# Performance work log

Hardware: AMD Instinct MI355X
Metric: run time of the kernel (lower is better)

Reference implementation:

```python
import jax, jax.numpy as jnp
import numpy as np

EPS = 1e-5

def _ln(x):
    # LayerNorm over last dim, no affine (elementwise_affine=False)
    mu = jnp.mean(x, axis=-1, keepdims=True)
    var = jnp.mean(jnp.square(x - mu), axis=-1, keepdims=True)
    return (x - mu) * jax.lax.rsqrt(var + EPS)

def setup_inputs() -> dict:
    key = jax.random.key(0)
    ks = jax.random.split(key, 6)
    B, L, D = 2, 2048, 2048
    s = 1.0 / np.sqrt(D)
    return {
        "x": jax.random.normal(ks[0], (B, L, D), jnp.float32),
        "Wq": jax.random.normal(ks[1], (D, D), jnp.float32) * s,
        "Wk": jax.random.normal(ks[2], (D, D), jnp.float32) * s,
        "Wv": jax.random.normal(ks[3], (D, D), jnp.float32) * s,
        "Wo": jax.random.normal(ks[4], (D, D), jnp.float32) * s,
        "bo": jnp.zeros((D,), jnp.float32),
    }

def reference(x, Wq, Wk, Wv, Wo, bo):
    B, L, D = x.shape
    H = 16
    hd = D // H
    q = (x @ Wq.T).reshape(B, L, H, hd)
    k = (x @ Wk.T).reshape(B, L, H, hd)
    v = (x @ Wv.T).reshape(B, L, H, hd)
    q = _ln(q)
    k = _ln(k)
    scores = jnp.einsum('blhd,bshd->bhls', q, k) / np.sqrt(hd)
    causal = jnp.tril(jnp.ones((L, L), bool))  # [L, L]
    scores = jnp.where(causal[None, None], scores, -jnp.inf)
    probs = jax.nn.softmax(scores, axis=-1)
    out = jnp.einsum('bhls,bshd->blhd', probs, v).reshape(B, L, D)
    return out @ Wo.T + bo
```

## Files before the change

### kernel.cpp

```cpp
#include <hip/hip_runtime.h>
#include <stdint.h>

typedef unsigned short u16;
typedef __attribute__((ext_vector_type(8))) unsigned short u16x8;
typedef __attribute__((ext_vector_type(8))) __bf16 bf16x8;
typedef __attribute__((ext_vector_type(4))) float f32x4;
typedef __attribute__((ext_vector_type(8))) float f32x8;

#define AS_G __attribute__((address_space(1)))
#define AS_L __attribute__((address_space(3)))

static __device__ __forceinline__ void gload_lds16(const u16* g, u16* l) {
  __builtin_amdgcn_global_load_lds((AS_G void*)(u16*)g, (AS_L void*)l, 16, 0, 0);
}

static __device__ __forceinline__ u16 f2bf(float f) {
  union { float f; unsigned u; } v; v.f = f;
  return (u16)((v.u + 0x7FFFu + ((v.u >> 16) & 1u)) >> 16);
}
static __device__ __forceinline__ float bf2f(u16 b) {
  union { unsigned u; float f; } v; v.u = ((unsigned)b) << 16;
  return v.f;
}
static __device__ __forceinline__ u16 f2bf_trunc(float f) {
  union { float f; unsigned u; } v; v.f = f;
  return (u16)(v.u >> 16);
}

#define BAR() do { asm volatile("" ::: "memory"); __builtin_amdgcn_s_barrier(); asm volatile("" ::: "memory"); } while (0)

__global__ __launch_bounds__(256) void cast_all(
    const float* __restrict__ x, const float* __restrict__ Wq,
    const float* __restrict__ Wk, const float* __restrict__ Wv,
    const float* __restrict__ Wo,
    u16* __restrict__ xb, u16* __restrict__ Wcat, u16* __restrict__ Wob)
{
  const int NX = (4096 * 2048) / 8;
  const int NW = (2048 * 2048) / 8;
  const int total = NX + 4 * NW;
  for (int i = blockIdx.x * 256 + threadIdx.x; i < total; i += gridDim.x * 256) {
    const float* src; u16* dst; int idx;
    if (i < NX)               { src = x;  dst = xb;                 idx = i; }
    else if (i < NX + NW)     { src = Wq; dst = Wcat;               idx = i - NX; }
    else if (i < NX + 2*NW)   { src = Wk; dst = Wcat + 2048*2048;   idx = i - NX - NW; }
    else if (i < NX + 3*NW)   { src = Wv; dst = Wcat + 2*2048*2048; idx = i - NX - 2*NW; }
    else                      { src = Wo; dst = Wob;                idx = i - NX - 3*NW; }
    f32x8 v = *(const f32x8*)(src + (size_t)idx * 8);
    u16x8 o;
    #pragma unroll
    for (int e = 0; e < 8; e++) o[e] = f2bf(v[e]);
    *(u16x8*)(dst + (size_t)idx * 8) = o;
  }
}

__global__ __launch_bounds__(512, 1) void gemm_qkv(
    const u16* __restrict__ A, const u16* __restrict__ B,
    u16* __restrict__ QK, u16* __restrict__ Vt, int K)
{
  __shared__ char SM[98304];
  u16* Asb = (u16*)SM;
  u16* Bsb = (u16*)(SM + 32768);
  const int tid = threadIdx.x, lane = tid & 63, wid = tid >> 6;
  const int wm = wid >> 2, wn = wid & 3;
  const int row0 = blockIdx.x * 128, col0 = blockIdx.y * 256;
  const int NT = K >> 6;

  const int sr  = tid >> 3;
  const int scb = ((tid & 7) * 16) ^ ((sr & 7) << 4);

  auto stA = [&](int buf, int t, int u) {
    const u16* src = A + (size_t)(row0 + u * 64 + sr) * K + t * 64 + (scb >> 1);
    gload_lds16(src, Asb + buf * 8192 + u * 4096 + wid * 512);
  };
  auto stB = [&](int buf, int t, int u) {
    const u16* src = B + (size_t)(col0 + u * 64 + sr) * K + t * 64 + (scb >> 1);
    gload_lds16(src, Bsb + buf * 16384 + u * 4096 + wid * 512);
  };
  auto ldA = [&](int buf, int mf, int k) {
    int ra = wm * 64 + mf * 16 + (lane & 15);
    int bc = (k * 64 + ((lane >> 4) << 4)) ^ ((ra & 7) << 4);
    return *(const bf16x8*)((const char*)Asb + buf * 16384 + ra * 128 + bc);
  };
  auto ldB = [&](int buf, int nf, int k) {
    int rb = wn * 64 + nf * 16 + (lane & 15);
    int bc = (k * 64 + ((lane >> 4) << 4)) ^ ((rb & 7) << 4);
    return *(const bf16x8*)((const char*)Bsb + buf * 32768 + rb * 128 + bc);
  };

  f32x4 acc[4][4] = {};
  bf16x8 breg[4][2];

#define MFMA_PH(mf, x0, x1) \
  do { __builtin_amdgcn_s_setprio(1); \
    _Pragma("unroll") \
    for (int nf = 0; nf < 4; ++nf) { \
      acc[mf][nf] = __builtin_amdgcn_mfma_f32_16x16x32_bf16(x0, breg[nf][0], acc[mf][nf], 0, 0, 0); \
      acc[mf][nf] = __builtin_amdgcn_mfma_f32_16x16x32_bf16(x1, breg[nf][1], acc[mf][nf], 0, 0, 0); \
    } \
    __builtin_amdgcn_s_setprio(0); } while (0)

  stA(0, 0, 0); stA(0, 0, 1);
  stB(0, 0, 0); stB(0, 0, 1); stB(0, 0, 2); stB(0, 0, 3);
  stB(1, 1, 0); stB(1, 1, 1); stB(1, 1, 2); stB(1, 1, 3);
  asm volatile("s_waitcnt vmcnt(4)" ::: "memory");
  BAR();

  for (int it = 0; it < NT / 2; ++it) {
    const int t1  = 2 * it + 1;
    const int pf0 = (2 * it + 2 < NT) ? (2 * it + 2) : (NT - 1);
    const int pf1 = (2 * it + 3 < NT) ? (2 * it + 3) : (NT - 1);
    #pragma unroll
    for (int hf = 0; hf < 2; ++hf) {
      const int cb = hf;
      #pragma unroll
      for (int nf = 0; nf < 4; ++nf) { breg[nf][0] = ldB(cb, nf, 0); breg[nf][1] = ldB(cb, nf, 1); }
      bf16x8 a0 = ldA(cb, 0, 0), a1 = ldA(cb, 0, 1);
      BAR();
      if (hf == 0) { stA(1, t1, 0); stA(1, t1, 1); } else { stA(0, pf0, 0); stA(0, pf0, 1); }
      MFMA_PH(0, a0, a1);
      a0 = ldA(cb, 1, 0); a1 = ldA(cb, 1, 1);
      BAR();
      if (hf == 0) { stB(0, pf0, 0); stB(0, pf0, 1); } else { stB(1, pf1, 0); stB(1, pf1, 1); }
      MFMA_PH(1, a0, a1);
      a0 = ldA(cb, 2, 0); a1 = ldA(cb, 2, 1);
      BAR();
      if (hf == 0) { stB(0, pf0, 2); stB(0, pf0, 3); } else { stB(1, pf1, 2); stB(1, pf1, 3); }
      MFMA_PH(2, a0, a1);
      a0 = ldA(cb, 3, 0); a1 = ldA(cb, 3, 1);
      MFMA_PH(3, a0, a1);
      asm volatile("s_waitcnt vmcnt(4)" ::: "memory");
      BAR();
    }
  }
  asm volatile("s_waitcnt vmcnt(0)" ::: "memory");
  BAR();

  if (col0 < 4096) {
    float* red = (float*)SM;
    #pragma unroll
    for (int mf = 0; mf < 4; ++mf) {
      #pragma unroll
      for (int e = 0; e < 4; ++e) {
        float s = acc[mf][0][e] + acc[mf][1][e] + acc[mf][2][e] + acc[mf][3][e];
        float q = acc[mf][0][e]*acc[mf][0][e] + acc[mf][1][e]*acc[mf][1][e]
                + acc[mf][2][e]*acc[mf][2][e] + acc[mf][3][e]*acc[mf][3][e];
        #pragma unroll
        for (int m = 1; m < 16; m <<= 1) { s += __shfl_xor(s, m); q += __shfl_xor(q, m); }
        if ((lane & 15) == 0) {
          int rl = mf * 16 + (lane >> 4) * 4 + e;
          red[wid * 128 + rl * 2]     = s;
          red[wid * 128 + rl * 2 + 1] = q;
        }
      }
    }
    BAR();
    const float mul = (col0 < 2048) ? (0.08838834764831845f * 1.4426950408889634f) : 1.0f;
    #pragma unroll
    for (int mf = 0; mf < 4; ++mf) {
      #pragma unroll
      for (int e = 0; e < 4; ++e) {
        int rl = mf * 16 + (lane >> 4) * 4 + e;
        float s = red[wid * 128 + rl * 2]     + red[(wid ^ 1) * 128 + rl * 2];
        float q = red[wid * 128 + rl * 2 + 1] + red[(wid ^ 1) * 128 + rl * 2 + 1];
        float mu = s * (1.f / 128.f);
        float var = q * (1.f / 128.f) - mu * mu;
        float rstd = rsqrtf(var + 1e-5f) * mul;
        int r = row0 + wm * 64 + rl;
        #pragma unroll
        for (int nf = 0; nf < 4; ++nf) {
          int c = col0 + wn * 64 + nf * 16 + (lane & 15);
          QK[(size_t)r * 4096 + c] = f2bf((acc[mf][nf][e] - mu) * rstd);
        }
      }
    }
  } else {
    u16* T = (u16*)SM;
    #pragma unroll
    for (int mf = 0; mf < 4; ++mf) {
      #pragma unroll
      for (int nf = 0; nf < 4; ++nf) {
        #pragma unroll
        for (int e = 0; e < 4; ++e) {
          int r = wm * 64 + mf * 16 + (lane >> 4) * 4 + e;
          int c = wn * 64 + nf * 16 + (lane & 15);
          T[c * 136 + r] = f2bf(acc[mf][nf][e]);
        }
      }
    }
    BAR();
    const int dr = tid >> 1, half = tid & 1;
    const int dg = col0 - 4096 + dr;
    const int h = dg >> 7, dd = dg & 127;
    const int b = row0 >> 11;
    const int lb = (row0 & 2047) + half * 64;
    u16* dst = Vt + ((size_t)((b * 16 + h) * 128 + dd)) * 2048 + lb;
    const u16* srcT = T + dr * 136 + half * 64;
    #pragma unroll
    for (int j = 0; j < 8; ++j)
      *(u16x8*)(dst + j * 8) = *(const u16x8*)(srcT + j * 8);
  }
#undef MFMA_PH
}

__global__ __launch_bounds__(512, 2) void gemm_ao(
    const u16* __restrict__ A, const u16* __restrict__ B,
    float* __restrict__ C, const float* __restrict__ bias,
    int M, int N, int K)
{
  __shared__ u16 As[2][256 * 64];
  __shared__ u16 Bs[2][128 * 64];
  const int tid = threadIdx.x, lane = tid & 63, wid = tid >> 6;
  const int wm = wid >> 1, wn = wid & 1;
  const int row0 = blockIdx.y * 256, col0 = blockIdx.x * 128;
  const int NT = K >> 6;

  const int sr  = tid >> 3;
  const int scb = ((tid & 7) * 16) ^ ((sr & 7) << 4);

  auto stA = [&](int buf, int t, int u) {
    const u16* src = A + (size_t)(row0 + u * 64 + sr) * K + t * 64 + (scb >> 1);
    gload_lds16(src, As[buf] + u * 4096 + wid * 512);
  };
  auto stB = [&](int buf, int t, int u) {
    const u16* src = B + (size_t)(col0 + u * 64 + sr) * K + t * 64 + (scb >> 1);
    gload_lds16(src, Bs[buf] + u * 4096 + wid * 512);
  };
  auto ldA = [&](int buf, int mf, int k) {
    int ra = wm * 64 + mf * 16 + (lane & 15);
    int bc = (k * 64 + ((lane >> 4) << 4)) ^ ((ra & 7) << 4);
    return *(const bf16x8*)((const char*)As[buf] + ra * 128 + bc);
  };
  auto ldB = [&](int buf, int nf, int k) {
    int rb = wn * 64 + nf * 16 + (lane & 15);
    int bc = (k * 64 + ((lane >> 4) << 4)) ^ ((rb & 7) << 4);
    return *(const bf16x8*)((const char*)Bs[buf] + rb * 128 + bc);
  };

  f32x4 acc[4][4] = {};
  bf16x8 breg[4][2];

  stA(0, 0, 0); stA(0, 0, 1); stA(0, 0, 2); stA(0, 0, 3);
  stB(0, 0, 0); stB(0, 0, 1);
  stB(1, 1, 0); stB(1, 1, 1);
  asm volatile("s_waitcnt vmcnt(2)" ::: "memory");
  BAR();

  for (int it = 0; it < NT / 2; ++it) {
    const int t1  = 2 * it + 1;
    const int pf0 = (2 * it + 2 < NT) ? (2 * it + 2) : (NT - 1);
    const int pf1 = (2 * it + 3 < NT) ? (2 * it + 3) : (NT - 1);
    #pragma unroll
    for (int hf = 0; hf < 2; ++hf) {
      const int cb = hf;
      #pragma unroll
      for (int nf = 0; nf < 4; ++nf) { breg[nf][0] = ldB(cb, nf, 0); breg[nf][1] = ldB(cb, nf, 1); }
      bf16x8 a0 = ldA(cb, 0, 0), a1 = ldA(cb, 0, 1);
      BAR();
      if (hf == 0) { stA(1, t1, 0); stA(1, t1, 1); } else { stA(0, pf0, 0); stA(0, pf0, 1); }
      __builtin_amdgcn_s_setprio(1);
      #pragma unroll
      for (int nf = 0; nf < 4; ++nf) {
        acc[0][nf] = __builtin_amdgcn_mfma_f32_16x16x32_bf16(a0, breg[nf][0], acc[0][nf], 0, 0, 0);
        acc[0][nf] = __builtin_amdgcn_mfma_f32_16x16x32_bf16(a1, breg[nf][1], acc[0][nf], 0, 0, 0);
      }
      __builtin_amdgcn_s_setprio(0);
      bf16x8 b0 = ldA(cb, 1, 0), b1 = ldA(cb, 1, 1);
      bf16x8 c0 = ldA(cb, 2, 0), c1 = ldA(cb, 2, 1);
      BAR();
      if (hf == 0) { stA(1, t1, 2); stA(1, t1, 3); } else { stA(0, pf0, 2); stA(0, pf0, 3); }
      __builtin_amdgcn_s_setprio(1);
      #pragma unroll
      for (int nf = 0; nf < 4; ++nf) {
        acc[1][nf] = __builtin_amdgcn_mfma_f32_16x16x32_bf16(b0, breg[nf][0], acc[1][nf], 0, 0, 0);
        acc[1][nf] = __builtin_amdgcn_mfma_f32_16x16x32_bf16(b1, breg[nf][1], acc[1][nf], 0, 0, 0);
        acc[2][nf] = __builtin_amdgcn_mfma_f32_16x16x32_bf16(c0, breg[nf][0], acc[2][nf], 0, 0, 0);
        acc[2][nf] = __builtin_amdgcn_mfma_f32_16x16x32_bf16(c1, breg[nf][1], acc[2][nf], 0, 0, 0);
      }
      __builtin_amdgcn_s_setprio(0);
      a0 = ldA(cb, 3, 0); a1 = ldA(cb, 3, 1);
      BAR();
      if (hf == 0) { stB(0, pf0, 0); stB(0, pf0, 1); } else { stB(1, pf1, 0); stB(1, pf1, 1); }
      __builtin_amdgcn_s_setprio(1);
      #pragma unroll
      for (int nf = 0; nf < 4; ++nf) {
        acc[3][nf] = __builtin_amdgcn_mfma_f32_16x16x32_bf16(a0, breg[nf][0], acc[3][nf], 0, 0, 0);
        acc[3][nf] = __builtin_amdgcn_mfma_f32_16x16x32_bf16(a1, breg[nf][1], acc[3][nf], 0, 0, 0);
      }
      __builtin_amdgcn_s_setprio(0);
      asm volatile("s_waitcnt vmcnt(2)" ::: "memory");
      BAR();
    }
  }
  asm volatile("s_waitcnt vmcnt(0)" ::: "memory");

  #pragma unroll
  for (int mf = 0; mf < 4; ++mf) {
    #pragma unroll
    for (int nf = 0; nf < 4; ++nf) {
      #pragma unroll
      for (int e = 0; e < 4; ++e) {
        int r = row0 + wm * 64 + mf * 16 + (lane >> 4) * 4 + e;
        int c = col0 + wn * 64 + nf * 16 + (lane & 15);
        C[(size_t)r * N + c] = acc[mf][nf][e] + bias[c];
      }
    }
  }
}

static __device__ __forceinline__ void stage_k_tile(
    const u16* __restrict__ QK, int b, int h, int j0, u16* Kbuf, int tid, int wid)
{
  #pragma unroll
  for (int i = 0; i < 4; i++) {
    int c = i * 256 + tid;
    int r = c >> 4, ob = (c & 15) * 16;
    int cb = ob ^ ((r & 7) << 4);
    const u16* g = QK + (size_t)(b*2048 + j0 + r) * 4096 + 2048 + h*128 + (cb >> 1);
    gload_lds16(g, Kbuf + (i * 256 + wid * 64) * 8);
  }
}
static __device__ __forceinline__ void stage_v_tile(
    const u16* __restrict__ Vt, int b, int h, int j0, u16* Vbuf, int tid, int wid)
{
  #pragma unroll
  for (int i = 0; i < 4; i++) {
    int c = i * 256 + tid;
    int r = c >> 3, ob = (c & 7) * 16;
    int cb = ob ^ ((r & 7) << 4);
    const u16* g = Vt + (size_t)((b*16 + h) * 128 + r) * 2048 + j0 + (cb >> 1);
    gload_lds16(g, Vbuf + (i * 256 + wid * 64) * 8);
  }
}

__global__ __launch_bounds__(256) void attn(
    const u16* __restrict__ QK, const u16* __restrict__ Vt, u16* __restrict__ AO)
{
  const int flat = blockIdx.x + (blockIdx.y << 4) + (blockIdx.z << 8);
  const int swz = (flat & 7) * 64 + (flat >> 3);
  const int pair = swz & 15;
  const int h = (swz >> 4) & 15;
  const int b = swz >> 8;
  const int tid = threadIdx.x, lane = tid & 63, wid = tid >> 6;

  __shared__ u16 Ks[2][64 * 128];
  __shared__ u16 Vs[2][128 * 64];
  __shared__ u16 Ps[4][16 * 64];

  for (int side = 0; side < 2; side++) {
    const int pp = side ? (31 - pair) : pair;
    const int l0 = pp * 64;
    const int ntile = pp + 1;

    bf16x8 qa[4];
    const u16* qrow = QK + (size_t)(b*2048 + l0 + wid*16 + (lane & 15)) * 4096
                      + h*128 + (lane >> 4) * 8;
    #pragma unroll
    for (int ks = 0; ks < 4; ks++) qa[ks] = *(const bf16x8*)(qrow + ks * 32);

    f32x4 o[8] = {};
    float mrun[4] = {-1e30f, -1e30f, -1e30f, -1e30f};
    float lrun[4] = {};

    stage_v_tile(Vt, b, h, 0, Vs[0], tid, wid);
    stage_k_tile(QK, b, h, 0, Ks[0], tid, wid);
    int cur = 0;

    for (int t = 0; t < ntile; t++) {
      if (t + 1 < ntile) {
        stage_v_tile(Vt, b, h, (t + 1) * 64, Vs[cur ^ 1], tid, wid);
        stage_k_tile(QK, b, h, (t + 1) * 64, Ks[cur ^ 1], tid, wid);
        asm volatile("s_waitcnt vmcnt(8)" ::: "memory");
      } else {
        asm volatile("s_waitcnt vmcnt(0)" ::: "memory");
      }
      __builtin_amdgcn_s_barrier();
      asm volatile("" ::: "memory");

      f32x4 s[4] = {};
      const char* Kc = (const char*)Ks[cur];
      __builtin_amdgcn_s_setprio(1);
      #pragma unroll
      for (int nt = 0; nt < 4; nt++) {
        #pragma unroll
        for (int ks = 0; ks < 4; ks++) {
          int r = nt * 16 + (lane & 15);
          int cb = ks * 64 + (lane >> 4) * 16;
          bf16x8 kb = *(const bf16x8*)(Kc + r * 256 + (cb ^ ((lane & 7) << 4)));
          s[nt] = __builtin_amdgcn_mfma_f32_16x16x32_bf16(qa[ks], kb, s[nt], 0, 0, 0);
        }
      }
      __builtin_amdgcn_s_setprio(0);

      if (t == ntile - 1) {
        #pragma unroll
        for (int nt = 0; nt < 4; nt++) {
          #pragma unroll
          for (int e = 0; e < 4; e++) {
            int i_loc = wid * 16 + (lane >> 4) * 4 + e;
            int j_loc = nt * 16 + (lane & 15);
            if (j_loc > i_loc) s[nt][e] = -1e30f;
          }
        }
      }

      float pmax[4];
      #pragma unroll
      for (int e = 0; e < 4; e++) {
        float v = fmaxf(fmaxf(s[0][e], s[1][e]), fmaxf(s[2][e], s[3][e]));
        v = fmaxf(v, __shfl_xor(v, 1));
        v = fmaxf(v, __shfl_xor(v, 2));
        v = fmaxf(v, __shfl_xor(v, 4));
        v = fmaxf(v, __shfl_xor(v, 8));
        pmax[e] = v;
      }
      bool need = (pmax[0] > mrun[0] + 8.f) || (pmax[1] > mrun[1] + 8.f) ||
                  (pmax[2] > mrun[2] + 8.f) || (pmax[3] > mrun[3] + 8.f);
      if (__any(need)) {
        float alpha[4];
        #pragma unroll
        for (int e = 0; e < 4; e++) {
          float mi = fmaxf(mrun[e], pmax[e]);
          alpha[e] = exp2f(mrun[e] - mi);
          mrun[e] = mi;
          lrun[e] *= alpha[e];
        }
        #pragma unroll
        for (int dt = 0; dt < 8; dt++)
          #pragma unroll
          for (int e = 0; e < 4; e++)
            o[dt][e] *= alpha[e];
      }

      char* PsW = (char*)Ps[wid];
      #pragma unroll
      for (int nt = 0; nt < 4; nt++) {
        #pragma unroll
        for (int e = 0; e < 4; e++) {
          float p = exp2f(s[nt][e] - mrun[e]);
          lrun[e] += p;
          int i_ = (lane >> 4) * 4 + e;
          int jb = (nt * 16 + (lane & 15)) * 2;
          *(u16*)(PsW + i_ * 128 + (jb ^ ((i_ & 7) << 4))) = f2bf_trunc(p);
        }
      }

      const char* Vc = (const char*)Vs[cur];
      __builtin_amdgcn_s_setprio(1);
      #pragma unroll
      for (int ks = 0; ks < 2; ks++) {
        int ir = lane & 15;
        int jb = ks * 64 + (lane >> 4) * 16;
        bf16x8 pa = *(const bf16x8*)(PsW + ir * 128 + (jb ^ ((ir & 7) << 4)));
        #pragma unroll
        for (int dt = 0; dt < 8; dt++) {
          int dr = dt * 16 + (lane & 15);
          bf16x8 vb = *(const bf16x8*)(Vc + dr * 128 + (jb ^ ((lane & 7) << 4)));
          o[dt] = __builtin_amdgcn_mfma_f32_16x16x32_bf16(pa, vb, o[dt], 0, 0, 0);
        }
      }
      __builtin_amdgcn_s_setprio(0);

      asm volatile("s_waitcnt lgkmcnt(0)" ::: "memory");
      __builtin_amdgcn_s_barrier();
      asm volatile("" ::: "memory");
      cur ^= 1;
    }

    #pragma unroll
    for (int e = 0; e < 4; e++) {
      float l = lrun[e];
      l += __shfl_xor(l, 1);
      l += __shfl_xor(l, 2);
      l += __shfl_xor(l, 4);
      l += __shfl_xor(l, 8);
      float inv = 1.0f / l;
      int rglob = b * 2048 + l0 + wid * 16 + (lane >> 4) * 4 + e;
      #pragma unroll
      for (int dt = 0; dt < 8; dt++)
        AO[(size_t)rglob * 2048 + h * 128 + dt * 16 + (lane & 15)] = f2bf(o[dt][e] * inv);
    }
  }
}

extern "C" void kernel_launch(void* const* d_in, const int* in_sizes, int n_in,
                              void* d_out, int out_size, void* d_ws, size_t ws_size,
                              hipStream_t stream)
{
  const float* x  = (const float*)d_in[0];
  const float* Wq = (const float*)d_in[1];
  const float* Wk = (const float*)d_in[2];
  const float* Wv = (const float*)d_in[3];
  const float* Wo = (const float*)d_in[4];
  const float* bo = (const float*)d_in[5];

  char* ws = (char*)d_ws;
  u16* xb   = (u16*)(ws);
  u16* Wcat = (u16*)(ws + 16777216);
  u16* Wob  = (u16*)(ws + 16777216 + 25165824);
  u16* QK   = (u16*)(ws + 16777216 + 25165824 + 8388608);
  u16* Vt   = (u16*)(ws + 16777216 + 25165824 + 8388608 + 33554432);
  u16* AO   = xb;

  cast_all<<<dim3(2048), dim3(256), 0, stream>>>(x, Wq, Wk, Wv, Wo, xb, Wcat, Wob);
  gemm_qkv<<<dim3(32, 24), dim3(512), 0, stream>>>(xb, Wcat, QK, Vt, 2048);
  attn<<<dim3(16, 16, 2), dim3(256), 0, stream>>>(QK, Vt, AO);
  gemm_ao<<<dim3(16, 16), dim3(512), 0, stream>>>(AO, Wob, (float*)d_out, bo, 4096, 2048, 2048);
}
```

Measured before the change: 258.9 us.

## Enlarge attention query tile to 128 rows per block for K/V reuse

The attention kernel now processes 128 query rows per block (32 per wave, two MFMA row tiles), so each staged K/V tile feeds twice as many MFMAs and global/LDS traffic per FLOP falls. The grid shrinks to 256 blocks with a simpler pair-to-block mapping, and waves whose rows are fully masked in the last tile skip it. The cost is higher register pressure (two accumulator sets, launch_bounds min 2 blocks) and half as many blocks, which may reduce occupancy and load balance across CUs.

```diff
diff --git a/kernel.cpp b/kernel.cpp
--- a/kernel.cpp
+++ b/kernel.cpp
@@ -332,40 +332,44 @@
   }
 }
 
-__global__ __launch_bounds__(256) void attn(
+__global__ __launch_bounds__(256, 2) void attn(
     const u16* __restrict__ QK, const u16* __restrict__ Vt, u16* __restrict__ AO)
 {
-  const int flat = blockIdx.x + (blockIdx.y << 4) + (blockIdx.z << 8);
-  const int swz = (flat & 7) * 64 + (flat >> 3);
-  const int pair = swz & 15;
-  const int h = (swz >> 4) & 15;
-  const int b = swz >> 8;
+  const int flat = blockIdx.x;
+  const int pair = flat >> 5;
+  const int hb   = flat & 31;
+  const int h = hb & 15, b = hb >> 4;
   const int tid = threadIdx.x, lane = tid & 63, wid = tid >> 6;
 
   __shared__ u16 Ks[2][64 * 128];
   __shared__ u16 Vs[2][128 * 64];
-  __shared__ u16 Ps[4][16 * 64];
+  __shared__ u16 Ps[4][32 * 64];
 
   for (int side = 0; side < 2; side++) {
-    const int pp = side ? (31 - pair) : pair;
-    const int l0 = pp * 64;
-    const int ntile = pp + 1;
-
-    bf16x8 qa[4];
-    const u16* qrow = QK + (size_t)(b*2048 + l0 + wid*16 + (lane & 15)) * 4096
-                      + h*128 + (lane >> 4) * 8;
-    #pragma unroll
-    for (int ks = 0; ks < 4; ks++) qa[ks] = *(const bf16x8*)(qrow + ks * 32);
-
-    f32x4 o[8] = {};
-    float mrun[4] = {-1e30f, -1e30f, -1e30f, -1e30f};
-    float lrun[4] = {};
+    const int pp = side ? (15 - pair) : pair;
+    const int l0 = pp * 128;
+    const int ntile = 2 * pp + 2;
+
+    bf16x8 qa[2][4];
+    #pragma unroll
+    for (int mt = 0; mt < 2; mt++) {
+      const u16* qrow = QK + (size_t)(b*2048 + l0 + wid*32 + mt*16 + (lane & 15)) * 4096
+                        + h*128 + (lane >> 4) * 8;
+      #pragma unroll
+      for (int ks = 0; ks < 4; ks++) qa[mt][ks] = *(const bf16x8*)(qrow + ks * 32);
+    }
+
+    f32x4 o[2][8] = {};
+    float mrun[8], lrun[8];
+    #pragma unroll
+    for (int i = 0; i < 8; i++) { mrun[i] = -1e30f; lrun[i] = 0.f; }
 
     stage_v_tile(Vt, b, h, 0, Vs[0], tid, wid);
     stage_k_tile(QK, b, h, 0, Ks[0], tid, wid);
     int cur = 0;
 
     for (int t = 0; t < ntile; t++) {
+      const int j0 = t * 64;
       if (t + 1 < ntile) {
         stage_v_tile(Vt, b, h, (t + 1) * 64, Vs[cur ^ 1], tid, wid);
         stage_k_tile(QK, b, h, (t + 1) * 64, Ks[cur ^ 1], tid, wid);
@@ -376,89 +380,108 @@
       __builtin_amdgcn_s_barrier();
       asm volatile("" ::: "memory");
 
-      f32x4 s[4] = {};
-      const char* Kc = (const char*)Ks[cur];
-      __builtin_amdgcn_s_setprio(1);
-      #pragma unroll
-      for (int nt = 0; nt < 4; nt++) {
-        #pragma unroll
-        for (int ks = 0; ks < 4; ks++) {
-          int r = nt * 16 + (lane & 15);
-          int cb = ks * 64 + (lane >> 4) * 16;
-          bf16x8 kb = *(const bf16x8*)(Kc + r * 256 + (cb ^ ((lane & 7) << 4)));
-          s[nt] = __builtin_amdgcn_mfma_f32_16x16x32_bf16(qa[ks], kb, s[nt], 0, 0, 0);
-        }
-      }
-      __builtin_amdgcn_s_setprio(0);
-
-      if (t == ntile - 1) {
+      const bool skip = (t == ntile - 1) && (wid < 2);
+      if (!skip) {
+        f32x4 s[2][4] = {};
+        const char* Kc = (const char*)Ks[cur];
+        __builtin_amdgcn_s_setprio(1);
         #pragma unroll
         for (int nt = 0; nt < 4; nt++) {
           #pragma unroll
+          for (int ks = 0; ks < 4; ks++) {
+            int r = nt * 16 + (lane & 15);
+            int cb = ks * 64 + (lane >> 4) * 16;
+            bf16x8 kb = *(const bf16x8*)(Kc + r * 256 + (cb ^ ((lane & 7) << 4)));
+            s[0][nt] = __builtin_amdgcn_mfma_f32_16x16x32_bf16(qa[0][ks], kb, s[0][nt], 0, 0, 0);
+            s[1][nt] = __builtin_amdgcn_mfma_f32_16x16x32_bf16(qa[1][ks], kb, s[1][nt], 0, 0, 0);
+          }
+        }
+        __builtin_amdgcn_s_setprio(0);
+
+        if (t >= ntile - 2) {
+          #pragma unroll
+          for (int mt = 0; mt < 2; mt++) {
+            #pragma unroll
+            for (int nt = 0; nt < 4; nt++) {
+              #pragma unroll
+              for (int e = 0; e < 4; e++) {
+                int ig = l0 + wid * 32 + mt * 16 + (lane >> 4) * 4 + e;
+                int jg = j0 + nt * 16 + (lane & 15);
+                if (jg > ig) s[mt][nt][e] = -1e30f;
+              }
+            }
+          }
+        }
+
+        float pmax[8];
+        #pragma unroll
+        for (int mt = 0; mt < 2; mt++) {
+          #pragma unroll
           for (int e = 0; e < 4; e++) {
-            int i_loc = wid * 16 + (lane >> 4) * 4 + e;
-            int j_loc = nt * 16 + (lane & 15);
-            if (j_loc > i_loc) s[nt][e] = -1e30f;
-          }
-        }
-      }
-
-      float pmax[4];
-      #pragma unroll
-      for (int e = 0; e < 4; e++) {
-        float v = fmaxf(fmaxf(s[0][e], s[1][e]), fmaxf(s[2][e], s[3][e]));
-        v = fmaxf(v, __shfl_xor(v, 1));
-        v = fmaxf(v, __shfl_xor(v, 2));
-        v = fmaxf(v, __shfl_xor(v, 4));
-        v = fmaxf(v, __shfl_xor(v, 8));
-        pmax[e] = v;
-      }
-      bool need = (pmax[0] > mrun[0] + 8.f) || (pmax[1] > mrun[1] + 8.f) ||
-                  (pmax[2] > mrun[2] + 8.f) || (pmax[3] > mrun[3] + 8.f);
-      if (__any(need)) {
-        float alpha[4];
-        #pragma unroll
-        for (int e = 0; e < 4; e++) {
-          float mi = fmaxf(mrun[e], pmax[e]);
-          alpha[e] = exp2f(mrun[e] - mi);
-          mrun[e] = mi;
-          lrun[e] *= alpha[e];
-        }
-        #pragma unroll
-        for (int dt = 0; dt < 8; dt++)
-          #pragma unroll
-          for (int e = 0; e < 4; e++)
-            o[dt][e] *= alpha[e];
-      }
-
-      char* PsW = (char*)Ps[wid];
-      #pragma unroll
-      for (int nt = 0; nt < 4; nt++) {
-        #pragma unroll
-        for (int e = 0; e < 4; e++) {
-          float p = exp2f(s[nt][e] - mrun[e]);
-          lrun[e] += p;
-          int i_ = (lane >> 4) * 4 + e;
-          int jb = (nt * 16 + (lane & 15)) * 2;
-          *(u16*)(PsW + i_ * 128 + (jb ^ ((i_ & 7) << 4))) = f2bf_trunc(p);
-        }
-      }
-
-      const char* Vc = (const char*)Vs[cur];
-      __builtin_amdgcn_s_setprio(1);
-      #pragma unroll
-      for (int ks = 0; ks < 2; ks++) {
-        int ir = lane & 15;
-        int jb = ks * 64 + (lane >> 4) * 16;
-        bf16x8 pa = *(const bf16x8*)(PsW + ir * 128 + (jb ^ ((ir & 7) << 4)));
-        #pragma unroll
-        for (int dt = 0; dt < 8; dt++) {
-          int dr = dt * 16 + (lane & 15);
-          bf16x8 vb = *(const bf16x8*)(Vc + dr * 128 + (jb ^ ((lane & 7) << 4)));
-          o[dt] = __builtin_amdgcn_mfma_f32_16x16x32_bf16(pa, vb, o[dt], 0, 0, 0);
-        }
-      }
-      __builtin_amdgcn_s_setprio(0);
+            float v = fmaxf(fmaxf(s[mt][0][e], s[mt][1][e]), fmaxf(s[mt][2][e], s[mt][3][e]));
+            v = fmaxf(v, __shfl_xor(v, 1));
+            v = fmaxf(v, __shfl_xor(v, 2));
+            v = fmaxf(v, __shfl_xor(v, 4));
+            v = fmaxf(v, __shfl_xor(v, 8));
+            pmax[mt * 4 + e] = v;
+          }
+        }
+        bool need = false;
+        #pragma unroll
+        for (int i = 0; i < 8; i++) need = need || (pmax[i] > mrun[i] + 8.f);
+        if (__any(need)) {
+          #pragma unroll
+          for (int mt = 0; mt < 2; mt++) {
+            #pragma unroll
+            for (int e = 0; e < 4; e++) {
+              int i = mt * 4 + e;
+              float mi = fmaxf(mrun[i], pmax[i]);
+              float alpha = exp2f(mrun[i] - mi);
+              mrun[i] = mi;
+              lrun[i] *= alpha;
+              #pragma unroll
+              for (int dt = 0; dt < 8; dt++) o[mt][dt][e] *= alpha;
+            }
+          }
+        }
+
+        char* PsW = (char*)Ps[wid];
+        #pragma unroll
+        for (int mt = 0; mt < 2; mt++) {
+          #pragma unroll
+          for (int nt = 0; nt < 4; nt++) {
+            #pragma unroll
+            for (int e = 0; e < 4; e++) {
+              float p = exp2f(s[mt][nt][e] - mrun[mt * 4 + e]);
+              lrun[mt * 4 + e] += p;
+              int i_ = mt * 16 + (lane >> 4) * 4 + e;
+              int jb = (nt * 16 + (lane & 15)) * 2;
+              *(u16*)(PsW + i_ * 128 + (jb ^ ((i_ & 7) << 4))) = f2bf_trunc(p);
+            }
+          }
+        }
+
+        const char* Vc = (const char*)Vs[cur];
+        __builtin_amdgcn_s_setprio(1);
+        #pragma unroll
+        for (int ks = 0; ks < 2; ks++) {
+          int jb = ks * 64 + (lane >> 4) * 16;
+          bf16x8 pa[2];
+          #pragma unroll
+          for (int mt = 0; mt < 2; mt++) {
+            int ir = mt * 16 + (lane & 15);
+            pa[mt] = *(const bf16x8*)(PsW + ir * 128 + (jb ^ ((ir & 7) << 4)));
+          }
+          #pragma unroll
+          for (int dt = 0; dt < 8; dt++) {
+            int dr = dt * 16 + (lane & 15);
+            bf16x8 vb = *(const bf16x8*)(Vc + dr * 128 + (jb ^ ((lane & 7) << 4)));
+            o[0][dt] = __builtin_amdgcn_mfma_f32_16x16x32_bf16(pa[0], vb, o[0][dt], 0, 0, 0);
+            o[1][dt] = __builtin_amdgcn_mfma_f32_16x16x32_bf16(pa[1], vb, o[1][dt], 0, 0, 0);
+          }
+        }
+        __builtin_amdgcn_s_setprio(0);
+      }
 
       asm volatile("s_waitcnt lgkmcnt(0)" ::: "memory");
       __builtin_amdgcn_s_barrier();
@@ -467,17 +490,20 @@
     }
 
     #pragma unroll
-    for (int e = 0; e < 4; e++) {
-      float l = lrun[e];
-      l += __shfl_xor(l, 1);
-      l += __shfl_xor(l, 2);
-      l += __shfl_xor(l, 4);
-      l += __shfl_xor(l, 8);
-      float inv = 1.0f / l;
-      int rglob = b * 2048 + l0 + wid * 16 + (lane >> 4) * 4 + e;
-      #pragma unroll
-      for (int dt = 0; dt < 8; dt++)
-        AO[(size_t)rglob * 2048 + h * 128 + dt * 16 + (lane & 15)] = f2bf(o[dt][e] * inv);
+    for (int mt = 0; mt < 2; mt++) {
+      #pragma unroll
+      for (int e = 0; e < 4; e++) {
+        float l = lrun[mt * 4 + e];
+        l += __shfl_xor(l, 1);
+        l += __shfl_xor(l, 2);
+        l += __shfl_xor(l, 4);
+        l += __shfl_xor(l, 8);
+        float inv = 1.0f / l;
+        int rglob = b * 2048 + l0 + wid * 32 + mt * 16 + (lane >> 4) * 4 + e;
+        #pragma unroll
+        for (int dt = 0; dt < 8; dt++)
+          AO[(size_t)rglob * 2048 + h * 128 + dt * 16 + (lane & 15)] = f2bf(o[mt][dt][e] * inv);
+      }
     }
   }
 }
@@ -503,6 +529,6 @@
 
   cast_all<<<dim3(2048), dim3(256), 0, stream>>>(x, Wq, Wk, Wv, Wo, xb, Wcat, Wob);
   gemm_qkv<<<dim3(32, 24), dim3(512), 0, stream>>>(xb, Wcat, QK, Vt, 2048);
-  attn<<<dim3(16, 16, 2), dim3(256), 0, stream>>>(QK, Vt, AO);
+  attn<<<dim3(256), dim3(256), 0, stream>>>(QK, Vt, AO);
   gemm_ao<<<dim3(16, 16), dim3(512), 0, stream>>>(AO, Wob, (float*)d_out, bo, 4096, 2048, 2048);
 }
```

New measurement: 284.2 us. +9.8%, slower.
